# Kernel tuning notes

Hardware: AMD Instinct MI355X
Metric: run time of the kernel (lower is better)

Reference implementation:

```python
import jax, jax.numpy as jnp
import numpy as np

B = 256
N_FACTS = 20
LQ = 16
LF = 16
E = 128
H = 256
DICT = 50000
GIN = 3 * H + 40  # 808
G_OUT = 256
F_OUT = 32


def setup_inputs() -> dict:
    key = jax.random.key(0)
    ks = iter(jax.random.split(key, 32))
    def w(shape, s=0.05):
        return jax.random.normal(next(ks), shape, jnp.float32) * s
    inp = {}
    inp["question_batch"] = jax.random.randint(next(ks), (B, LQ), 0, DICT + 1)
    inp["facts_batch"] = jax.random.randint(next(ks), (B * N_FACTS, LF), 0, DICT + 1)
    inp["embedding"] = w((DICT + 1, E))
    for nm in ("q", "f"):
        inp[f"Wih_{nm}"] = w((4 * H, E))
        inp[f"Whh_{nm}"] = w((4 * H, H))
        inp[f"bih_{nm}"] = jnp.zeros((4 * H,), jnp.float32)
        inp[f"bhh_{nm}"] = jnp.zeros((4 * H,), jnp.float32)
    g_dims = [GIN, 256, 256, 256, G_OUT]
    for i in range(4):
        inp[f"g_W{i}"] = w((g_dims[i + 1], g_dims[i]))
        inp[f"g_b{i}"] = jnp.zeros((g_dims[i + 1],), jnp.float32)
    f_dims = [G_OUT, 256, 512, F_OUT]
    for i in range(3):
        inp[f"f_W{i}"] = w((f_dims[i + 1], f_dims[i]))
        inp[f"f_b{i}"] = jnp.zeros((f_dims[i + 1],), jnp.float32)
    return inp


def lstm_final_hidden(x, Wih, Whh, bih, bhh):
    # x: [N, T, E] -> final hidden state h_T: [N, H] (PyTorch gate order i,f,g,o)
    n = x.shape[0]
    h0 = jnp.zeros((n, H), x.dtype)
    c0 = jnp.zeros((n, H), x.dtype)
    def step(carry, xt):
        h, c = carry
        gates = xt @ Wih.T + h @ Whh.T + bih + bhh  # [N, 4H]
        i, f, g, o = jnp.split(gates, 4, axis=-1)
        i = jax.nn.sigmoid(i); f = jax.nn.sigmoid(f); o = jax.nn.sigmoid(o)
        g = jnp.tanh(g)
        c = f * c + i * g
        h = o * jnp.tanh(c)
        return (h, c), None
    (h, c), _ = jax.lax.scan(step, (h0, c0), jnp.swapaxes(x, 0, 1))
    return h


def mlp(x, Ws, bs):
    # relu after every layer incl. output (mlp_tanh=False), dropout off (eval)
    for W, b in zip(Ws, bs):
        x = jax.nn.relu(x @ W.T + b)
    return x


def reference(question_batch, facts_batch, embedding,
              Wih_q, Whh_q, bih_q, bhh_q,
              Wih_f, Whh_f, bih_f, bhh_f,
              g_W0, g_b0, g_W1, g_b1, g_W2, g_b2, g_W3, g_b3,
              f_W0, f_b0, f_W1, f_b1, f_W2, f_b2):
    q_emb = embedding[question_batch]          # [B, LQ, E]
    f_emb = embedding[facts_batch]             # [B*N, LF, E]
    qh = lstm_final_hidden(q_emb, Wih_q, Whh_q, bih_q, bhh_q)   # [B, H]
    fh = lstm_final_hidden(f_emb, Wih_f, Whh_f, bih_f, bhh_f)   # [B*N, H]
    fh = fh.reshape(B, N_FACTS, H)
    sep = jnp.eye(20, dtype=fh.dtype)[:N_FACTS]                 # [N, 20]
    fh = jnp.concatenate([fh, jnp.broadcast_to(sep, (B, N_FACTS, 20))], axis=2)  # [B, N, H+20]
    # pairwise: oi cycles facts fast, oj repeats each fact N times (matches torch repeat/view)
    oi = jnp.tile(fh, (1, N_FACTS, 1))                           # [B, N*N, H+20]
    oj = jnp.repeat(fh, N_FACTS, axis=1)                         # [B, N*N, H+20]
    qr = jnp.broadcast_to(qh[:, None, :], (B, N_FACTS * N_FACTS, H))
    pair = jnp.concatenate([oi, oj, qr], axis=2)                 # [B, N*N, 3H+40]
    rel = mlp(pair.reshape(-1, GIN), (g_W0, g_W1, g_W2, g_W3), (g_b0, g_b1, g_b2, g_b3))
    rel_sum = rel.reshape(B, N_FACTS * N_FACTS, G_OUT).sum(axis=1)  # [B, G_OUT]
    out = mlp(rel_sum, (f_W0, f_W1, f_W2), (f_b0, f_b1, f_b2))      # [B, F_OUT]
    return out
```

## Files before the change

### kernel.cpp

```cpp
#include <hip/hip_runtime.h>
#include <math.h>

typedef __attribute__((ext_vector_type(8))) short short8;
typedef __attribute__((ext_vector_type(4))) float f32x4;
typedef __attribute__((ext_vector_type(4))) unsigned short u16x4;

#define NBQ 256
#define NBF 5120
#define MROWS 5376
#define E_ 128
#define H_ 256
#define DICTP1 50001
#define GIN_ 808
#define CH_ROWS 51200
#define CH_B 128
#define NCHUNK 2

__device__ __forceinline__ unsigned short f2bf(float x) {
    unsigned int u = __float_as_uint(x);
    u += 0x7fffu + ((u >> 16) & 1u);
    return (unsigned short)(u >> 16);
}
__device__ __forceinline__ float bf2f(unsigned short b) {
    return __uint_as_float(((unsigned int)b) << 16);
}
__device__ __forceinline__ float sigmoidf_(float x) { return 1.0f / (1.0f + expf(-x)); }

__device__ __forceinline__ void gload16(const void* g, void* l) {
    __builtin_amdgcn_global_load_lds((const __attribute__((address_space(1))) void*)g,
                                     (__attribute__((address_space(3))) void*)l, 16, 0, 0);
}
__device__ __forceinline__ short8 lds_frag(const unsigned char* base, int row, int ko) {
    const int off = (row << 7) + ((ko << 1) ^ ((row & 7) << 4));
    return *reinterpret_cast<const short8*>(base + off);
}

template <int RELU, int OBF>
__global__ __launch_bounds__(256) void mm_bf16(
    const unsigned short* __restrict__ A, int lda,
    const unsigned short* __restrict__ B, int ldb,
    const float* __restrict__ bias,
    float* __restrict__ Cf, unsigned short* __restrict__ Cb, int ldc, int K)
{
    __shared__ __align__(16) unsigned char Ash[16384];
    __shared__ __align__(16) unsigned char Bsh[16384];
    const int tid = threadIdx.x, lane = tid & 63, widx = tid >> 6;
    const int wr = widx >> 1, wc = widx & 1;
    const int gr = blockIdx.x * 128, gc = blockIdx.y * 128;
    const int rsub = lane >> 3, cgrp = lane & 7;
    f32x4 acc[4][4] = {};
    for (int kt = 0; kt < K; kt += 64) {
        #pragma unroll
        for (int j = 0; j < 4; ++j) {
            const int ch = (widx << 2) + j;
            const int r = (ch << 3) + rsub;
            const int ce = (cgrp ^ (r & 7)) << 3;
            gload16(A + (size_t)(gr + r) * lda + kt + ce, Ash + (ch << 10));
            gload16(B + (size_t)(gc + r) * ldb + kt + ce, Bsh + (ch << 10));
        }
        __syncthreads();
        #pragma unroll
        for (int kk = 0; kk < 64; kk += 32) {
            const int ko = kk + ((lane >> 4) << 3);
            short8 af[4], bfr[4];
            #pragma unroll
            for (int i = 0; i < 4; ++i) {
                af[i]  = lds_frag(Ash, wr * 64 + i * 16 + (lane & 15), ko);
                bfr[i] = lds_frag(Bsh, wc * 64 + i * 16 + (lane & 15), ko);
            }
            #pragma unroll
            for (int mi = 0; mi < 4; ++mi)
                #pragma unroll
                for (int ni = 0; ni < 4; ++ni)
                    acc[mi][ni] = __builtin_amdgcn_mfma_f32_16x16x32_bf16(af[mi], bfr[ni], acc[mi][ni], 0, 0, 0);
        }
        __syncthreads();
    }
    const int rq = (lane >> 4) << 2, cl = lane & 15;
    #pragma unroll
    for (int ni = 0; ni < 4; ++ni) {
        const int n = gc + wc * 64 + ni * 16 + cl;
        const float bv = bias ? bias[n] : 0.f;
        #pragma unroll
        for (int mi = 0; mi < 4; ++mi) {
            #pragma unroll
            for (int rg = 0; rg < 4; ++rg) {
                const int m = gr + wr * 64 + mi * 16 + rq + rg;
                float v = acc[mi][ni][rg] + bv;
                if (RELU) v = fmaxf(v, 0.f);
                if (OBF) Cb[(size_t)m * ldc + n] = f2bf(v);
                else     Cf[(size_t)m * ldc + n] = v;
            }
        }
    }
}

__global__ __launch_bounds__(256) void lstm_step(
    const int* __restrict__ qidx, const int* __restrict__ fidx,
    const unsigned short* __restrict__ embb,
    const unsigned short* __restrict__ Wq, const unsigned short* __restrict__ Wf,
    const float* __restrict__ bsq, const float* __restrict__ bsf,
    const unsigned short* __restrict__ hr, unsigned short* __restrict__ hw,
    float* __restrict__ c, int t)
{
    __shared__ __align__(16) unsigned char Ash[16384];
    __shared__ __align__(16) unsigned char Bsh[16384];
    const int tid = threadIdx.x, lane = tid & 63, widx = tid >> 6;
    const int wr = widx >> 1, wc = widx & 1;
    const int gr = blockIdx.x * 128, bc = blockIdx.y;
    const bool isq = (gr < NBQ);
    const unsigned short* W = isq ? Wq : Wf;
    const float* bs = isq ? bsq : bsf;
    const int rsub = lane >> 3, cgrp = lane & 7;
    f32x4 acc[4][4] = {};
    for (int kt = 0; kt < 384; kt += 64) {
        #pragma unroll
        for (int j = 0; j < 4; ++j) {
            const int ch = (widx << 2) + j;
            const int r = (ch << 3) + rsub;
            const int ce = (cgrp ^ (r & 7)) << 3;
            const int n = gr + r;
            const unsigned short* asrc;
            if (kt < E_) {
                const int tok = isq ? qidx[(n << 4) + t] : fidx[((n - NBQ) << 4) + t];
                asrc = embb + (size_t)tok * E_ + kt + ce;
            } else {
                asrc = hr + (size_t)n * H_ + (kt - E_) + ce;
            }
            gload16(asrc, Ash + (ch << 10));
            const int grow = (((r & 63) >> 4) << 8) + (bc << 5) + ((r >> 6) << 4) + (r & 15);
            gload16(W + (size_t)grow * 384 + kt + ce, Bsh + (ch << 10));
        }
        __syncthreads();
        #pragma unroll
        for (int kk = 0; kk < 64; kk += 32) {
            const int ko = kk + ((lane >> 4) << 3);
            short8 af[4], bfr[4];
            #pragma unroll
            for (int i = 0; i < 4; ++i) {
                af[i]  = lds_frag(Ash, wr * 64 + i * 16 + (lane & 15), ko);
                bfr[i] = lds_frag(Bsh, wc * 64 + i * 16 + (lane & 15), ko);
            }
            #pragma unroll
            for (int mi = 0; mi < 4; ++mi)
                #pragma unroll
                for (int ni = 0; ni < 4; ++ni)
                    acc[mi][ni] = __builtin_amdgcn_mfma_f32_16x16x32_bf16(af[mi], bfr[ni], acc[mi][ni], 0, 0, 0);
        }
        __syncthreads();
    }
    const int hcol = (bc << 5) + (wc << 4) + (lane & 15);
    float bsv[4];
    #pragma unroll
    for (int g = 0; g < 4; ++g) bsv[g] = bs[(g << 8) + hcol];
    #pragma unroll
    for (int mi = 0; mi < 4; ++mi) {
        #pragma unroll
        for (int rg = 0; rg < 4; ++rg) {
            const int m = gr + wr * 64 + mi * 16 + ((lane >> 4) << 2) + rg;
            const float iv = sigmoidf_(acc[mi][0][rg] + bsv[0]);
            const float fv = sigmoidf_(acc[mi][1][rg] + bsv[1]);
            const float gv = tanhf(acc[mi][2][rg] + bsv[2]);
            const float ov = sigmoidf_(acc[mi][3][rg] + bsv[3]);
            const size_t idx = (size_t)m * H_ + hcol;
            const float cn = fv * c[idx] + iv * gv;
            c[idx] = cn;
            hw[idx] = f2bf(ov * tanhf(cn));
        }
    }
}

__global__ void cvt_bf16(const float* __restrict__ s, unsigned short* __restrict__ d, int n) {
    for (int i = blockIdx.x * blockDim.x + threadIdx.x; i < n; i += gridDim.x * blockDim.x)
        d[i] = f2bf(s[i]);
}

__global__ void pack_lstm_w(const float* __restrict__ Wih, const float* __restrict__ Whh,
                            const float* __restrict__ bih, const float* __restrict__ bhh,
                            unsigned short* __restrict__ Wc, float* __restrict__ bsum) {
    const int r = blockIdx.x;
    const int cx = threadIdx.x;
    const float v = (cx < E_) ? Wih[r * E_ + cx] : Whh[r * H_ + cx - E_];
    Wc[r * 384 + cx] = f2bf(v);
    if (cx == 0) bsum[r] = bih[r] + bhh[r];
}

__global__ __launch_bounds__(256) void pack_w0(const float* __restrict__ gW0, const float* __restrict__ gb0,
                                               unsigned short* __restrict__ W0ab, unsigned short* __restrict__ W0c,
                                               float* __restrict__ sepU, float* __restrict__ sepV) {
    const int idx = blockIdx.x * 256 + threadIdx.x;
    if (idx < 131072) {
        const int r = idx >> 8, cc = idx & 255;
        const float v = (r < 256) ? gW0[(size_t)r * GIN_ + cc] : gW0[(size_t)(r - 256) * GIN_ + 276 + cc];
        W0ab[idx] = f2bf(v);
    } else if (idx < 196608) {
        const int l = idx - 131072;
        const int r = l >> 8, cc = l & 255;
        W0c[l] = f2bf(gW0[(size_t)r * GIN_ + 552 + cc]);
    } else if (idx < 201728) {
        const int l = idx - 196608;
        const int i = l >> 8, j = l & 255;
        sepU[l] = gW0[(size_t)j * GIN_ + 256 + i] + gb0[j];
    } else {
        const int l = idx - 201728;
        const int i = l >> 8, j = l & 255;
        sepV[l] = gW0[(size_t)j * GIN_ + 532 + i];
    }
}

__global__ __launch_bounds__(256) void rel0_kernel(
    const float* __restrict__ UV, const float* __restrict__ Q0,
    const float* __restrict__ sepU, const float* __restrict__ sepV,
    unsigned short* __restrict__ out, int row0)
{
    const int row = blockIdx.x * 4 + (threadIdx.x >> 6);
    const int k4 = (threadIdx.x & 63) << 2;
    const int grow = row0 + row;
    const int b = grow / 400;
    const int rem = grow - b * 400;
    const int oi = rem % 20, oj = rem / 20;
    const float4 u  = *(const float4*)(UV + (size_t)(b * 20 + oi) * 512 + k4);
    const float4 v  = *(const float4*)(UV + (size_t)(b * 20 + oj) * 512 + 256 + k4);
    const float4 q  = *(const float4*)(Q0 + (size_t)b * H_ + k4);
    const float4 su = *(const float4*)(sepU + oi * H_ + k4);
    const float4 sv = *(const float4*)(sepV + oj * H_ + k4);
    u16x4 o;
    o.x = f2bf(fmaxf(u.x + v.x + q.x + su.x + sv.x, 0.f));
    o.y = f2bf(fmaxf(u.y + v.y + q.y + su.y + sv.y, 0.f));
    o.z = f2bf(fmaxf(u.z + v.z + q.z + su.z + sv.z, 0.f));
    o.w = f2bf(fmaxf(u.w + v.w + q.w + su.w + sv.w, 0.f));
    *(u16x4*)(out + (size_t)row * H_ + k4) = o;
}

__global__ __launch_bounds__(256) void sum400(const unsigned short* __restrict__ rel,
                                              float* __restrict__ rel_sum, int b0)
{
    const int bl = blockIdx.x;
    const int k = threadIdx.x;
    const unsigned short* base = rel + (size_t)bl * 400 * H_ + k;
    float s = 0.f;
    #pragma unroll 4
    for (int p = 0; p < 400; ++p) s += bf2f(base[(size_t)p * H_]);
    rel_sum[(size_t)(b0 + bl) * H_ + k] = s;
}

template <int RELU>
__global__ __launch_bounds__(256) void gemm_nt(
    const float* __restrict__ A, int lda,
    const float* __restrict__ B, int ldb,
    const float* __restrict__ bias,
    float* __restrict__ C, int ldc,
    int M, int N, int K)
{
    __shared__ float As[16][68];
    __shared__ float Bs[16][68];
    const int tid = threadIdx.x;
    const int tx = tid & 15, ty = tid >> 4;
    const int lrow = tid >> 2;
    const int lk = (tid & 3) << 2;
    const int gr = blockIdx.x * 64, gc = blockIdx.y * 64;
    const int ar = gr + lrow;
    const int brr = gc + lrow;
    const float* __restrict__ arow = A + (size_t)ar * lda;
    const float* __restrict__ brow = B + (size_t)brr * ldb;
    const bool aval = ar < M, bval = brr < N;
    float acc[4][4] = {};
    for (int k0 = 0; k0 < K; k0 += 16) {
        float4 a4 = make_float4(0.f, 0.f, 0.f, 0.f), b4 = make_float4(0.f, 0.f, 0.f, 0.f);
        if (aval) a4 = *reinterpret_cast<const float4*>(arow + k0 + lk);
        if (bval) b4 = *reinterpret_cast<const float4*>(brow + k0 + lk);
        As[lk + 0][lrow] = a4.x; As[lk + 1][lrow] = a4.y; As[lk + 2][lrow] = a4.z; As[lk + 3][lrow] = a4.w;
        Bs[lk + 0][lrow] = b4.x; Bs[lk + 1][lrow] = b4.y; Bs[lk + 2][lrow] = b4.z; Bs[lk + 3][lrow] = b4.w;
        __syncthreads();
        #pragma unroll
        for (int kk = 0; kk < 16; ++kk) {
            float a0 = As[kk][ty * 4 + 0], a1 = As[kk][ty * 4 + 1], a2 = As[kk][ty * 4 + 2], a3 = As[kk][ty * 4 + 3];
            float b0 = Bs[kk][tx * 4 + 0], b1 = Bs[kk][tx * 4 + 1], b2 = Bs[kk][tx * 4 + 2], b3 = Bs[kk][tx * 4 + 3];
            acc[0][0] += a0 * b0; acc[0][1] += a0 * b1; acc[0][2] += a0 * b2; acc[0][3] += a0 * b3;
            acc[1][0] += a1 * b0; acc[1][1] += a1 * b1; acc[1][2] += a1 * b2; acc[1][3] += a1 * b3;
            acc[2][0] += a2 * b0; acc[2][1] += a2 * b1; acc[2][2] += a2 * b2; acc[2][3] += a2 * b3;
            acc[3][0] += a3 * b0; acc[3][1] += a3 * b1; acc[3][2] += a3 * b2; acc[3][3] += a3 * b3;
        }
        __syncthreads();
    }
    #pragma unroll
    for (int i = 0; i < 4; ++i)
        #pragma unroll
        for (int jj = 0; jj < 4; ++jj) {
            const int r = gr + ty * 4 + i, cc = gc + tx * 4 + jj;
            if (r < M && cc < N) {
                float v = acc[i][jj] + (bias ? bias[cc] : 0.f);
                if (RELU) v = fmaxf(v, 0.f);
                C[(size_t)r * ldc + cc] = v;
            }
        }
}

extern "C" void kernel_launch(void* const* d_in, const int* in_sizes, int n_in,
                              void* d_out, int out_size, void* d_ws, size_t ws_size,
                              hipStream_t stream)
{
    const int* qidx = (const int*)d_in[0];
    const int* fidx = (const int*)d_in[1];
    const float* emb = (const float*)d_in[2];
    const float* Wih_q = (const float*)d_in[3];
    const float* Whh_q = (const float*)d_in[4];
    const float* bih_q = (const float*)d_in[5];
    const float* bhh_q = (const float*)d_in[6];
    const float* Wih_f = (const float*)d_in[7];
    const float* Whh_f = (const float*)d_in[8];
    const float* bih_f = (const float*)d_in[9];
    const float* bhh_f = (const float*)d_in[10];
    const float* gW0 = (const float*)d_in[11];
    const float* gb0 = (const float*)d_in[12];
    const float* gW1 = (const float*)d_in[13];
    const float* gb1 = (const float*)d_in[14];
    const float* gW2 = (const float*)d_in[15];
    const float* gb2 = (const float*)d_in[16];
    const float* gW3 = (const float*)d_in[17];
    const float* gb3 = (const float*)d_in[18];
    const float* fW0 = (const float*)d_in[19];
    const float* fb0 = (const float*)d_in[20];
    const float* fW1 = (const float*)d_in[21];
    const float* fb1 = (const float*)d_in[22];
    const float* fW2 = (const float*)d_in[23];
    const float* fb2 = (const float*)d_in[24];
    float* out = (float*)d_out;

    char* w = (char*)d_ws;
    float* c = (float*)w;                    w += (size_t)MROWS * H_ * 4;
    unsigned short* hb0 = (unsigned short*)w; w += (size_t)MROWS * H_ * 2;
    unsigned short* hb1 = (unsigned short*)w; w += (size_t)MROWS * H_ * 2;
    unsigned short* embb = (unsigned short*)w; w += (size_t)DICTP1 * E_ * 2;
    unsigned short* Wq = (unsigned short*)w;  w += (size_t)1024 * 384 * 2;
    unsigned short* Wf = (unsigned short*)w;  w += (size_t)1024 * 384 * 2;
    float* bsq = (float*)w;                  w += 1024 * 4;
    float* bsf = (float*)w;                  w += 1024 * 4;
    unsigned short* W0ab = (unsigned short*)w; w += (size_t)512 * 256 * 2;
    unsigned short* W0c = (unsigned short*)w;  w += (size_t)256 * 256 * 2;
    unsigned short* gw1b = (unsigned short*)w; w += (size_t)256 * 256 * 2;
    unsigned short* gw2b = (unsigned short*)w; w += (size_t)256 * 256 * 2;
    unsigned short* gw3b = (unsigned short*)w; w += (size_t)256 * 256 * 2;
    float* sepU = (float*)w;                 w += 20 * 256 * 4;
    float* sepV = (float*)w;                 w += 20 * 256 * 4;
    float* UV = (float*)w;                   w += (size_t)NBF * 512 * 4;
    float* Q0 = (float*)w;                   w += (size_t)NBQ * H_ * 4;
    unsigned short* rel_a = (unsigned short*)w; w += (size_t)CH_ROWS * H_ * 2;
    unsigned short* rel_b = (unsigned short*)w; w += (size_t)CH_ROWS * H_ * 2;
    float* rel_sum = (float*)w;              w += (size_t)NBQ * H_ * 4;
    float* fout1 = (float*)w;                w += (size_t)NBQ * 256 * 4;
    float* fout2 = (float*)w;                w += (size_t)NBQ * 512 * 4;

    hipMemsetAsync(c, 0, (size_t)MROWS * H_ * 4 + (size_t)MROWS * H_ * 2, stream);

    cvt_bf16<<<2048, 256, 0, stream>>>(emb, embb, DICTP1 * E_);
    pack_lstm_w<<<1024, 384, 0, stream>>>(Wih_q, Whh_q, bih_q, bhh_q, Wq, bsq);
    pack_lstm_w<<<1024, 384, 0, stream>>>(Wih_f, Whh_f, bih_f, bhh_f, Wf, bsf);
    pack_w0<<<808, 256, 0, stream>>>(gW0, gb0, W0ab, W0c, sepU, sepV);
    cvt_bf16<<<64, 256, 0, stream>>>(gW1, gw1b, 256 * 256);
    cvt_bf16<<<64, 256, 0, stream>>>(gW2, gw2b, 256 * 256);
    cvt_bf16<<<64, 256, 0, stream>>>(gW3, gw3b, 256 * 256);

    for (int t = 0; t < 16; ++t) {
        const unsigned short* hr = (t & 1) ? hb1 : hb0;
        unsigned short* hw = (t & 1) ? hb0 : hb1;
        lstm_step<<<dim3(MROWS / 128, 8), 256, 0, stream>>>(
            qidx, fidx, embb, Wq, Wf, bsq, bsf, hr, hw, c, t);
    }
    const unsigned short* hfin = hb0;

    const unsigned short* fh = hfin + (size_t)NBQ * H_;
    mm_bf16<0, 0><<<dim3(NBF / 128, 4), 256, 0, stream>>>(fh, H_, W0ab, H_, nullptr, UV, nullptr, 512, H_);
    mm_bf16<0, 0><<<dim3(NBQ / 128, 2), 256, 0, stream>>>(hfin, H_, W0c, H_, nullptr, Q0, nullptr, H_, H_);

    for (int ch = 0; ch < NCHUNK; ++ch) {
        const int row0 = ch * CH_ROWS;
        rel0_kernel<<<CH_ROWS / 4, 256, 0, stream>>>(UV, Q0, sepU, sepV, rel_a, row0);
        mm_bf16<1, 1><<<dim3(CH_ROWS / 128, 2), 256, 0, stream>>>(rel_a, H_, gw1b, H_, gb1, nullptr, rel_b, H_, H_);
        mm_bf16<1, 1><<<dim3(CH_ROWS / 128, 2), 256, 0, stream>>>(rel_b, H_, gw2b, H_, gb2, nullptr, rel_a, H_, H_);
        mm_bf16<1, 1><<<dim3(CH_ROWS / 128, 2), 256, 0, stream>>>(rel_a, H_, gw3b, H_, gb3, nullptr, rel_b, H_, H_);
        sum400<<<CH_B, 256, 0, stream>>>(rel_b, rel_sum, ch * CH_B);
    }

    gemm_nt<1><<<dim3(NBQ / 64, 256 / 64), 256, 0, stream>>>(rel_sum, H_, fW0, H_, fb0, fout1, H_, NBQ, 256, H_);
    gemm_nt<1><<<dim3(NBQ / 64, 512 / 64), 256, 0, stream>>>(fout1, 256, fW1, 256, fb1, fout2, 512, NBQ, 512, 256);
    gemm_nt<1><<<dim3(NBQ / 64, 1), 256, 0, stream>>>(fout2, 512, fW2, 512, fb2, out, 32, NBQ, 32, 512);
}
```

Before: 700.5 us.

## Fuse relation MLP layers and pair-sum into one LDS-resident kernel

Replaces the chunked pipeline (rel0 build, three separate GEMM launches writing bf16 activations to global, then sum400) with a single kernel. Each 32-row block builds its layer-0 activations in LDS, runs the three 256x256 layers keeping activations in shared memory, and reduces the final output into rel_sum with atomics split at batch boundaries. This removes the global round-trips of about 100K x 256 intermediate activations and several launches. In exchange, every block reloads the full weight matrices, the per-block M tile is small (32 rows), and atomic accumulation makes the summation order nondeterministic.

```diff
diff --git a/kernel.cpp b/kernel.cpp
--- a/kernel.cpp
+++ b/kernel.cpp
@@ -12,9 +12,6 @@
 #define H_ 256
 #define DICTP1 50001
 #define GIN_ 808
-#define CH_ROWS 51200
-#define CH_B 128
-#define NCHUNK 2
 
 __device__ __forceinline__ unsigned short f2bf(float x) {
     unsigned int u = __float_as_uint(x);
@@ -30,69 +27,11 @@
     __builtin_amdgcn_global_load_lds((const __attribute__((address_space(1))) void*)g,
                                      (__attribute__((address_space(3))) void*)l, 16, 0, 0);
 }
-__device__ __forceinline__ short8 lds_frag(const unsigned char* base, int row, int ko) {
-    const int off = (row << 7) + ((ko << 1) ^ ((row & 7) << 4));
-    return *reinterpret_cast<const short8*>(base + off);
-}
-
-template <int RELU, int OBF>
-__global__ __launch_bounds__(256) void mm_bf16(
-    const unsigned short* __restrict__ A, int lda,
-    const unsigned short* __restrict__ B, int ldb,
-    const float* __restrict__ bias,
-    float* __restrict__ Cf, unsigned short* __restrict__ Cb, int ldc, int K)
-{
-    __shared__ __align__(16) unsigned char Ash[16384];
-    __shared__ __align__(16) unsigned char Bsh[16384];
-    const int tid = threadIdx.x, lane = tid & 63, widx = tid >> 6;
-    const int wr = widx >> 1, wc = widx & 1;
-    const int gr = blockIdx.x * 128, gc = blockIdx.y * 128;
-    const int rsub = lane >> 3, cgrp = lane & 7;
-    f32x4 acc[4][4] = {};
-    for (int kt = 0; kt < K; kt += 64) {
-        #pragma unroll
-        for (int j = 0; j < 4; ++j) {
-            const int ch = (widx << 2) + j;
-            const int r = (ch << 3) + rsub;
-            const int ce = (cgrp ^ (r & 7)) << 3;
-            gload16(A + (size_t)(gr + r) * lda + kt + ce, Ash + (ch << 10));
-            gload16(B + (size_t)(gc + r) * ldb + kt + ce, Bsh + (ch << 10));
-        }
-        __syncthreads();
-        #pragma unroll
-        for (int kk = 0; kk < 64; kk += 32) {
-            const int ko = kk + ((lane >> 4) << 3);
-            short8 af[4], bfr[4];
-            #pragma unroll
-            for (int i = 0; i < 4; ++i) {
-                af[i]  = lds_frag(Ash, wr * 64 + i * 16 + (lane & 15), ko);
-                bfr[i] = lds_frag(Bsh, wc * 64 + i * 16 + (lane & 15), ko);
-            }
-            #pragma unroll
-            for (int mi = 0; mi < 4; ++mi)
-                #pragma unroll
-                for (int ni = 0; ni < 4; ++ni)
-                    acc[mi][ni] = __builtin_amdgcn_mfma_f32_16x16x32_bf16(af[mi], bfr[ni], acc[mi][ni], 0, 0, 0);
-        }
-        __syncthreads();
-    }
-    const int rq = (lane >> 4) << 2, cl = lane & 15;
-    #pragma unroll
-    for (int ni = 0; ni < 4; ++ni) {
-        const int n = gc + wc * 64 + ni * 16 + cl;
-        const float bv = bias ? bias[n] : 0.f;
-        #pragma unroll
-        for (int mi = 0; mi < 4; ++mi) {
-            #pragma unroll
-            for (int rg = 0; rg < 4; ++rg) {
-                const int m = gr + wr * 64 + mi * 16 + rq + rg;
-                float v = acc[mi][ni][rg] + bv;
-                if (RELU) v = fmaxf(v, 0.f);
-                if (OBF) Cb[(size_t)m * ldc + n] = f2bf(v);
-                else     Cf[(size_t)m * ldc + n] = v;
-            }
-        }
-    }
+__device__ __forceinline__ short8 frag128(const unsigned char* base, int row, int ko) {
+    return *reinterpret_cast<const short8*>(base + (row << 7) + ((ko << 1) ^ ((row & 7) << 4)));
+}
+__device__ __forceinline__ short8 frag512(const unsigned char* base, int row, int ko) {
+    return *reinterpret_cast<const short8*>(base + (row << 9) + ((ko << 1) ^ ((row & 7) << 4)));
 }
 
 __global__ __launch_bounds__(256) void lstm_step(
@@ -138,8 +77,8 @@
             short8 af[4], bfr[4];
             #pragma unroll
             for (int i = 0; i < 4; ++i) {
-                af[i]  = lds_frag(Ash, wr * 64 + i * 16 + (lane & 15), ko);
-                bfr[i] = lds_frag(Bsh, wc * 64 + i * 16 + (lane & 15), ko);
+                af[i]  = frag128(Ash, wr * 64 + i * 16 + (lane & 15), ko);
+                bfr[i] = frag128(Bsh, wc * 64 + i * 16 + (lane & 15), ko);
             }
             #pragma unroll
             for (int mi = 0; mi < 4; ++mi)
@@ -166,6 +105,183 @@
             const float cn = fv * c[idx] + iv * gv;
             c[idx] = cn;
             hw[idx] = f2bf(ov * tanhf(cn));
+        }
+    }
+}
+
+__global__ __launch_bounds__(256) void g123sum(
+    const float* __restrict__ UV, const float* __restrict__ Q0,
+    const float* __restrict__ sepU, const float* __restrict__ sepV,
+    const unsigned short* __restrict__ gw1b, const float* __restrict__ gb1,
+    const unsigned short* __restrict__ gw2b, const float* __restrict__ gb2,
+    const unsigned short* __restrict__ gw3b, const float* __restrict__ gb3,
+    float* __restrict__ rel_sum)
+{
+    __shared__ __align__(16) unsigned char actA[16384];
+    __shared__ __align__(16) unsigned char actB[16384];
+    __shared__ __align__(16) unsigned char Wsh[32768];
+    const int tid = threadIdx.x, lane = tid & 63, widx = tid >> 6;
+    const int grow0 = blockIdx.x << 5;
+    {
+        const int r = tid >> 3;
+        const int c0 = (tid & 7) << 5;
+        const int grow = grow0 + r;
+        const int b = grow / 400;
+        const int rem = grow - b * 400;
+        const int oi = rem % 20, oj = rem / 20;
+        const float* up = UV + ((size_t)(b * 20 + oi) << 9);
+        const float* vp = UV + ((size_t)(b * 20 + oj) << 9) + 256;
+        const float* qp = Q0 + ((size_t)b << 8);
+        const float* sup = sepU + (oi << 8);
+        const float* svp = sepV + (oj << 8);
+        #pragma unroll
+        for (int cc = 0; cc < 32; cc += 4) {
+            const int c = c0 + cc;
+            const float4 u = *(const float4*)(up + c);
+            const float4 v = *(const float4*)(vp + c);
+            const float4 q = *(const float4*)(qp + c);
+            const float4 su = *(const float4*)(sup + c);
+            const float4 sv = *(const float4*)(svp + c);
+            u16x4 pk;
+            pk.x = f2bf(fmaxf(u.x + v.x + q.x + su.x + sv.x, 0.f));
+            pk.y = f2bf(fmaxf(u.y + v.y + q.y + su.y + sv.y, 0.f));
+            pk.z = f2bf(fmaxf(u.z + v.z + q.z + su.z + sv.z, 0.f));
+            pk.w = f2bf(fmaxf(u.w + v.w + q.w + su.w + sv.w, 0.f));
+            *(u16x4*)(actA + (r << 9) + (((c << 1) ^ ((r & 7) << 4)))) = pk;
+        }
+    }
+    #pragma unroll 1
+    for (int L = 0; L < 3; ++L) {
+        const unsigned char* ain = (L & 1) ? actB : actA;
+        unsigned char* aout = (L & 1) ? actA : actB;
+        const unsigned short* Wp = (L == 0) ? gw1b : (L == 1) ? gw2b : gw3b;
+        const float* bl = (L == 0) ? gb1 : (L == 1) ? gb2 : gb3;
+        f32x4 acc[2][4] = {};
+        for (int kc = 0; kc < 4; ++kc) {
+            #pragma unroll
+            for (int j = 0; j < 8; ++j) {
+                const int unit = (widx << 3) + j;
+                const int r = (unit << 3) + (lane >> 3);
+                const int ce = ((lane & 7) ^ (r & 7)) << 3;
+                gload16(Wp + ((size_t)r << 8) + (kc << 6) + ce, Wsh + (unit << 10));
+            }
+            __syncthreads();
+            #pragma unroll
+            for (int ks = 0; ks < 2; ++ks) {
+                const int kof = (ks << 5) + ((lane >> 4) << 3);
+                const int kcol = (kc << 6) + kof;
+                short8 af[2], bfr[4];
+                af[0] = frag512(ain, (lane & 15), kcol);
+                af[1] = frag512(ain, 16 + (lane & 15), kcol);
+                #pragma unroll
+                for (int ni = 0; ni < 4; ++ni)
+                    bfr[ni] = frag128(Wsh, (widx << 6) + (ni << 4) + (lane & 15), kof);
+                #pragma unroll
+                for (int mi = 0; mi < 2; ++mi)
+                    #pragma unroll
+                    for (int ni = 0; ni < 4; ++ni)
+                        acc[mi][ni] = __builtin_amdgcn_mfma_f32_16x16x32_bf16(af[mi], bfr[ni], acc[mi][ni], 0, 0, 0);
+            }
+            __syncthreads();
+        }
+        float bv[4];
+        #pragma unroll
+        for (int ni = 0; ni < 4; ++ni) bv[ni] = bl[(widx << 6) + (ni << 4) + (lane & 15)];
+        if (L < 2) {
+            #pragma unroll
+            for (int mi = 0; mi < 2; ++mi)
+                #pragma unroll
+                for (int ni = 0; ni < 4; ++ni)
+                    #pragma unroll
+                    for (int rg4 = 0; rg4 < 4; ++rg4) {
+                        const float v = fmaxf(acc[mi][ni][rg4] + bv[ni], 0.f);
+                        const int row = (mi << 4) + ((lane >> 4) << 2) + rg4;
+                        const int col = (widx << 6) + (ni << 4) + (lane & 15);
+                        *(unsigned short*)(aout + (row << 9) + (((col << 1) ^ ((row & 7) << 4)))) = f2bf(v);
+                    }
+        } else {
+            const int bstart = grow0 / 400;
+            const int rsplit = (bstart + 1) * 400 - grow0;
+            const int b1 = (bstart < 255) ? bstart + 1 : 255;
+            #pragma unroll
+            for (int ni = 0; ni < 4; ++ni) {
+                float s0 = 0.f, s1 = 0.f;
+                #pragma unroll
+                for (int mi = 0; mi < 2; ++mi)
+                    #pragma unroll
+                    for (int rg4 = 0; rg4 < 4; ++rg4) {
+                        const int row = (mi << 4) + ((lane >> 4) << 2) + rg4;
+                        const float v = fmaxf(acc[mi][ni][rg4] + bv[ni], 0.f);
+                        if (row < rsplit) s0 += v; else s1 += v;
+                    }
+                s0 += __shfl_xor(s0, 16); s0 += __shfl_xor(s0, 32);
+                s1 += __shfl_xor(s1, 16); s1 += __shfl_xor(s1, 32);
+                if (lane < 16) {
+                    const int col = (widx << 6) + (ni << 4) + lane;
+                    atomicAdd(&rel_sum[(bstart << 8) + col], s0);
+                    atomicAdd(&rel_sum[(b1 << 8) + col], s1);
+                }
+            }
+        }
+    }
+}
+
+template <int RELU, int OBF>
+__global__ __launch_bounds__(256) void mm_bf16(
+    const unsigned short* __restrict__ A, int lda,
+    const unsigned short* __restrict__ B, int ldb,
+    const float* __restrict__ bias,
+    float* __restrict__ Cf, unsigned short* __restrict__ Cb, int ldc, int K)
+{
+    __shared__ __align__(16) unsigned char Ash[16384];
+    __shared__ __align__(16) unsigned char Bsh[16384];
+    const int tid = threadIdx.x, lane = tid & 63, widx = tid >> 6;
+    const int wr = widx >> 1, wc = widx & 1;
+    const int gr = blockIdx.x * 128, gc = blockIdx.y * 128;
+    const int rsub = lane >> 3, cgrp = lane & 7;
+    f32x4 acc[4][4] = {};
+    for (int kt = 0; kt < K; kt += 64) {
+        #pragma unroll
+        for (int j = 0; j < 4; ++j) {
+            const int ch = (widx << 2) + j;
+            const int r = (ch << 3) + rsub;
+            const int ce = (cgrp ^ (r & 7)) << 3;
+            gload16(A + (size_t)(gr + r) * lda + kt + ce, Ash + (ch << 10));
+            gload16(B + (size_t)(gc + r) * ldb + kt + ce, Bsh + (ch << 10));
+        }
+        __syncthreads();
+        #pragma unroll
+        for (int kk = 0; kk < 64; kk += 32) {
+            const int ko = kk + ((lane >> 4) << 3);
+            short8 af[4], bfr[4];
+            #pragma unroll
+            for (int i = 0; i < 4; ++i) {
+                af[i]  = frag128(Ash, wr * 64 + i * 16 + (lane & 15), ko);
+                bfr[i] = frag128(Bsh, wc * 64 + i * 16 + (lane & 15), ko);
+            }
+            #pragma unroll
+            for (int mi = 0; mi < 4; ++mi)
+                #pragma unroll
+                for (int ni = 0; ni < 4; ++ni)
+                    acc[mi][ni] = __builtin_amdgcn_mfma_f32_16x16x32_bf16(af[mi], bfr[ni], acc[mi][ni], 0, 0, 0);
+        }
+        __syncthreads();
+    }
+    const int rq = (lane >> 4) << 2, cl = lane & 15;
+    #pragma unroll
+    for (int ni = 0; ni < 4; ++ni) {
+        const int n = gc + wc * 64 + ni * 16 + cl;
+        const float bv = bias ? bias[n] : 0.f;
+        #pragma unroll
+        for (int mi = 0; mi < 4; ++mi) {
+            #pragma unroll
+            for (int rg = 0; rg < 4; ++rg) {
+                const int m = gr + wr * 64 + mi * 16 + rq + rg;
+                float v = acc[mi][ni][rg] + bv;
+                if (RELU) v = fmaxf(v, 0.f);
+                if (OBF) Cb[(size_t)m * ldc + n] = f2bf(v);
+                else     Cf[(size_t)m * ldc + n] = v;
+            }
         }
     }
 }
@@ -206,42 +322,6 @@
         const int i = l >> 8, j = l & 255;
         sepV[l] = gW0[(size_t)j * GIN_ + 532 + i];
     }
-}
-
-__global__ __launch_bounds__(256) void rel0_kernel(
-    const float* __restrict__ UV, const float* __restrict__ Q0,
-    const float* __restrict__ sepU, const float* __restrict__ sepV,
-    unsigned short* __restrict__ out, int row0)
-{
-    const int row = blockIdx.x * 4 + (threadIdx.x >> 6);
-    const int k4 = (threadIdx.x & 63) << 2;
-    const int grow = row0 + row;
-    const int b = grow / 400;
-    const int rem = grow - b * 400;
-    const int oi = rem % 20, oj = rem / 20;
-    const float4 u  = *(const float4*)(UV + (size_t)(b * 20 + oi) * 512 + k4);
-    const float4 v  = *(const float4*)(UV + (size_t)(b * 20 + oj) * 512 + 256 + k4);
-    const float4 q  = *(const float4*)(Q0 + (size_t)b * H_ + k4);
-    const float4 su = *(const float4*)(sepU + oi * H_ + k4);
-    const float4 sv = *(const float4*)(sepV + oj * H_ + k4);
-    u16x4 o;
-    o.x = f2bf(fmaxf(u.x + v.x + q.x + su.x + sv.x, 0.f));
-    o.y = f2bf(fmaxf(u.y + v.y + q.y + su.y + sv.y, 0.f));
-    o.z = f2bf(fmaxf(u.z + v.z + q.z + su.z + sv.z, 0.f));
-    o.w = f2bf(fmaxf(u.w + v.w + q.w + su.w + sv.w, 0.f));
-    *(u16x4*)(out + (size_t)row * H_ + k4) = o;
-}
-
-__global__ __launch_bounds__(256) void sum400(const unsigned short* __restrict__ rel,
-                                              float* __restrict__ rel_sum, int b0)
-{
-    const int bl = blockIdx.x;
-    const int k = threadIdx.x;
-    const unsigned short* base = rel + (size_t)bl * 400 * H_ + k;
-    float s = 0.f;
-    #pragma unroll 4
-    for (int p = 0; p < 400; ++p) s += bf2f(base[(size_t)p * H_]);
-    rel_sum[(size_t)(b0 + bl) * H_ + k] = s;
 }
 
 template <int RELU>
@@ -328,30 +408,29 @@
     float* out = (float*)d_out;
 
     char* w = (char*)d_ws;
-    float* c = (float*)w;                    w += (size_t)MROWS * H_ * 4;
-    unsigned short* hb0 = (unsigned short*)w; w += (size_t)MROWS * H_ * 2;
-    unsigned short* hb1 = (unsigned short*)w; w += (size_t)MROWS * H_ * 2;
+    float* c = (float*)w;                      w += (size_t)MROWS * H_ * 4;
+    unsigned short* hb0 = (unsigned short*)w;  w += (size_t)MROWS * H_ * 2;
+    unsigned short* hb1 = (unsigned short*)w;  w += (size_t)MROWS * H_ * 2;
     unsigned short* embb = (unsigned short*)w; w += (size_t)DICTP1 * E_ * 2;
-    unsigned short* Wq = (unsigned short*)w;  w += (size_t)1024 * 384 * 2;
-    unsigned short* Wf = (unsigned short*)w;  w += (size_t)1024 * 384 * 2;
-    float* bsq = (float*)w;                  w += 1024 * 4;
-    float* bsf = (float*)w;                  w += 1024 * 4;
+    unsigned short* Wq = (unsigned short*)w;   w += (size_t)1024 * 384 * 2;
+    unsigned short* Wf = (unsigned short*)w;   w += (size_t)1024 * 384 * 2;
+    float* bsq = (float*)w;                    w += 1024 * 4;
+    float* bsf = (float*)w;                    w += 1024 * 4;
     unsigned short* W0ab = (unsigned short*)w; w += (size_t)512 * 256 * 2;
     unsigned short* W0c = (unsigned short*)w;  w += (size_t)256 * 256 * 2;
     unsigned short* gw1b = (unsigned short*)w; w += (size_t)256 * 256 * 2;
     unsigned short* gw2b = (unsigned short*)w; w += (size_t)256 * 256 * 2;
     unsigned short* gw3b = (unsigned short*)w; w += (size_t)256 * 256 * 2;
-    float* sepU = (float*)w;                 w += 20 * 256 * 4;
-    float* sepV = (float*)w;                 w += 20 * 256 * 4;
-    float* UV = (float*)w;                   w += (size_t)NBF * 512 * 4;
-    float* Q0 = (float*)w;                   w += (size_t)NBQ * H_ * 4;
-    unsigned short* rel_a = (unsigned short*)w; w += (size_t)CH_ROWS * H_ * 2;
-    unsigned short* rel_b = (unsigned short*)w; w += (size_t)CH_ROWS * H_ * 2;
-    float* rel_sum = (float*)w;              w += (size_t)NBQ * H_ * 4;
-    float* fout1 = (float*)w;                w += (size_t)NBQ * 256 * 4;
-    float* fout2 = (float*)w;                w += (size_t)NBQ * 512 * 4;
-
-    hipMemsetAsync(c, 0, (size_t)MROWS * H_ * 4 + (size_t)MROWS * H_ * 2, stream);
+    float* sepU = (float*)w;                   w += 20 * 256 * 4;
+    float* sepV = (float*)w;                   w += 20 * 256 * 4;
+    float* UV = (float*)w;                     w += (size_t)NBF * 512 * 4;
+    float* Q0 = (float*)w;                     w += (size_t)NBQ * H_ * 4;
+    float* rel_sum = (float*)w;                w += (size_t)NBQ * H_ * 4;
+    float* fout1 = (float*)w;                  w += (size_t)NBQ * 256 * 4;
+    float* fout2 = (float*)w;                  w += (size_t)NBQ * 512 * 4;
+
+    (void)hipMemsetAsync(c, 0, (size_t)MROWS * H_ * 4 + (size_t)MROWS * H_ * 2, stream);
+    (void)hipMemsetAsync(rel_sum, 0, (size_t)NBQ * H_ * 4, stream);
 
     cvt_bf16<<<2048, 256, 0, stream>>>(emb, embb, DICTP1 * E_);
     pack_lstm_w<<<1024, 384, 0, stream>>>(Wih_q, Whh_q, bih_q, bhh_q, Wq, bsq);
@@ -367,20 +446,12 @@
         lstm_step<<<dim3(MROWS / 128, 8), 256, 0, stream>>>(
             qidx, fidx, embb, Wq, Wf, bsq, bsf, hr, hw, c, t);
     }
-    const unsigned short* hfin = hb0;
-
-    const unsigned short* fh = hfin + (size_t)NBQ * H_;
+
+    const unsigned short* fh = hb0 + (size_t)NBQ * H_;
     mm_bf16<0, 0><<<dim3(NBF / 128, 4), 256, 0, stream>>>(fh, H_, W0ab, H_, nullptr, UV, nullptr, 512, H_);
-    mm_bf16<0, 0><<<dim3(NBQ / 128, 2), 256, 0, stream>>>(hfin, H_, W0c, H_, nullptr, Q0, nullptr, H_, H_);
-
-    for (int ch = 0; ch < NCHUNK; ++ch) {
-        const int row0 = ch * CH_ROWS;
-        rel0_kernel<<<CH_ROWS / 4, 256, 0, stream>>>(UV, Q0, sepU, sepV, rel_a, row0);
-        mm_bf16<1, 1><<<dim3(CH_ROWS / 128, 2), 256, 0, stream>>>(rel_a, H_, gw1b, H_, gb1, nullptr, rel_b, H_, H_);
-        mm_bf16<1, 1><<<dim3(CH_ROWS / 128, 2), 256, 0, stream>>>(rel_b, H_, gw2b, H_, gb2, nullptr, rel_a, H_, H_);
-        mm_bf16<1, 1><<<dim3(CH_ROWS / 128, 2), 256, 0, stream>>>(rel_a, H_, gw3b, H_, gb3, nullptr, rel_b, H_, H_);
-        sum400<<<CH_B, 256, 0, stream>>>(rel_b, rel_sum, ch * CH_B);
-    }
+    mm_bf16<0, 0><<<dim3(NBQ / 128, 2), 256, 0, stream>>>(hb0, H_, W0c, H_, nullptr, Q0, nullptr, H_, H_);
+
+    g123sum<<<3200, 256, 0, stream>>>(UV, Q0, sepU, sepV, gw1b, gb1, gw2b, gb2, gw3b, gb3, rel_sum);
 
     gemm_nt<1><<<dim3(NBQ / 64, 256 / 64), 256, 0, stream>>>(rel_sum, H_, fW0, H_, fb0, fout1, H_, NBQ, 256, H_);
     gemm_nt<1><<<dim3(NBQ / 64, 512 / 64), 256, 0, stream>>>(fout1, 256, fW1, 256, fb1, fout2, 512, NBQ, 512, 256);
```

After: 635.5 us. -9.3%, faster.
